# Optimization experiments

Hardware: AMD Instinct MI355X
Metric: run time of the kernel (lower is better)

## Reference

```python
import jax, jax.numpy as jnp
import numpy as np
jax.config.update("jax_enable_x64", True)

WINDOW_SHAPE = (16, 16, 8)
SPARSE_SHAPE = (512, 512, 64)
GROUP_SIZE = 128
BATCH_COUNTS = np.array([500000, 480123, 510007, 495870], dtype=np.int64)  # not multiples of 128 -> padding path active


def setup_inputs() -> dict:
    key = jax.random.key(0)
    kx, ky, kz = jax.random.split(key, 3)
    N = int(BATCH_COUNTS.sum())
    bids = jnp.asarray(np.repeat(np.arange(len(BATCH_COUNTS), dtype=np.int64), BATCH_COUNTS))
    x = jax.random.randint(kx, (N,), 0, SPARSE_SHAPE[0], dtype=jnp.int64)
    y = jax.random.randint(ky, (N,), 0, SPARSE_SHAPE[1], dtype=jnp.int64)
    z = jax.random.randint(kz, (N,), 0, SPARSE_SHAPE[2], dtype=jnp.int64)
    coords = jnp.stack([bids, x, y, z], axis=1)  # [N,4] int64: (batch, x, y, z)
    return {"coords": coords, "batch_size": 4}


def _hash_keys(coords, shifted):
    n, m, l = SPARSE_SHAPE
    n2o, m2o, l2o = WINDOW_SHAPE
    n1 = int(np.ceil(n / n2o) + 1)
    m1 = int(np.ceil(m / m2o) + 1)
    l1 = int(np.ceil(l / l2o) + 1)
    if shifted:
        x = coords[:, 1] + n2o // 2
        y = coords[:, 2] + m2o // 2
        z = coords[:, 3] + l2o // 2
    else:
        x, y, z = coords[:, 1], coords[:, 2], coords[:, 3]
    x1, y1, z1 = x // n2o, y // m2o, z // l2o
    x2, y2, z2 = x % n2o, y % m2o, z % l2o
    # original code triples both window and grid-of-window extents before hashing
    n2, m2, l2 = 3 * n2o, 3 * m2o, 3 * l2o
    n1, m1, l1 = 3 * n1, 3 * m1, 3 * l1
    sx = 1 - 2 * (x1 & 1)  # (-1)**x1
    sy = 1 - 2 * (y1 & 1)
    sz = 1 - 2 * (z1 & 1)
    s2x = 1 - 2 * (x2 & 1)
    s2y = 1 - 2 * (y2 & 1)
    s2z = 1 - 2 * (z2 & 1)
    boff = coords[:, 0] * (n * m * l * 10)
    vx = (n1 * y1 + n1 * m1 * z1 + sy * x1) * (n2 * m2 * l2) + sy * (m2 * x2 + n2 * m2 * z2 + s2x * y2) + boff
    vy = (m1 * z1 + m1 * l1 * x1 + sz * y1) * (m2 * l2 * n2) + sz * (l2 * y2 + m2 * l2 * x2 + s2y * z2) + boff
    vz = (l1 * x1 + l1 * n1 * y1 + sx * z1) * (l2 * n2 * m2) + sx * (n2 * z2 + l2 * n2 * y2 + s2z * x2) + boff
    return vx, vy, vz


def reference(coords, batch_size):
    G = GROUP_SIZE
    coords = coords.astype(jnp.int64)
    bids = coords[:, 0]
    N = coords.shape[0]
    num_per_batch = jax.ops.segment_sum(jnp.ones((N,), jnp.int64), bids, num_segments=batch_size)
    bs = jnp.concatenate([jnp.zeros((1,), jnp.int64), jnp.cumsum(num_per_batch)])
    num_per_batch_p = ((num_per_batch + G - 1) // G) * G
    bsp = jnp.concatenate([jnp.zeros((1,), jnp.int64), jnp.cumsum(num_per_batch_p)])
    Np = int(bsp[-1])  # concrete (not under jit); padded total length

    # win2flat[j] = j + (bsp[b] - bs[b]) for b = batch of element j (coords assumed batch-sorted)
    win2flat = jnp.arange(N, dtype=jnp.int64) + (bsp[:-1] - bs[:-1])[bids]

    # flat2win: identity within each padded batch, with the padded tail replicated
    # from one group earlier, then shifted back to flat indexing.
    p = jnp.arange(Np, dtype=jnp.int64)
    b = jnp.searchsorted(bsp, p, side="right") - 1  # batch of each padded slot
    r = num_per_batch % G
    pad_tail = (r[b] != 0) & (p >= bsp[b + 1] - G + r[b])
    flat2win = p - G * pad_tail.astype(jnp.int64) - (bsp[b] - bs[b])

    outs = [flat2win, win2flat]
    for shifted in (False, True):
        vx, vy, vz = _hash_keys(coords, shifted)
        outs.append(jnp.argsort(vx))
        outs.append(jnp.argsort(vy))
        outs.append(jnp.argsort(vz))
    # (flat2win, win2flat, x, y, z, x_shift, y_shift, z_shift)
    return tuple(outs)
```

## Files before the change

### kernel.cpp

```cpp
#include <hip/hip_runtime.h>
#include <type_traits>

typedef unsigned long long u64;
typedef unsigned int u32;

#define BLOCK     256
#define WAVES     4
#define TILE      4096
#define SUBT      1024
#define CHUNKS    16
#define KSHIFT    21
#define KBIAS     (1LL << 21)
#define KMASK     ((1u << 21) - 1)
#define GRP       128


__device__ __forceinline__ void hash3(long long x, long long y, long long z,
                                      long long boff, long long* v) {
  long long x1 = x >> 4, y1 = y >> 4, z1 = z >> 3;
  long long x2 = x & 15, y2 = y & 15, z2 = z & 7;
  long long sx  = 1 - 2*(x1 & 1), sy  = 1 - 2*(y1 & 1), sz  = 1 - 2*(z1 & 1);
  long long s2x = 1 - 2*(x2 & 1), s2y = 1 - 2*(y2 & 1), s2z = 1 - 2*(z2 & 1);
  v[0] = (99*y1 + 9801*z1 + sy*x1)*55296 + sy*(48*x2 + 2304*z2 + s2x*y2) + boff;
  v[1] = (99*z1 + 2673*x1 + sz*y1)*55296 + sz*(24*y2 + 1152*x2 + s2y*z2) + boff;
  v[2] = (27*x1 + 2673*y1 + sx*z1)*55296 + sx*(48*z2 + 1152*y2 + s2z*x2) + boff;
}

__global__ void count_k(const int* __restrict__ coords, unsigned* __restrict__ counts, int N) {
  __shared__ unsigned c[8];
  if (threadIdx.x < 8) c[threadIdx.x] = 0;
  __syncthreads();
  for (int i = blockIdx.x*blockDim.x + threadIdx.x; i < N; i += gridDim.x*blockDim.x)
    atomicAdd(&c[coords[4*i] & 7], 1u);
  __syncthreads();
  if (threadIdx.x < 8) atomicAdd(&counts[threadIdx.x], c[threadIdx.x]);
}

__global__ void prefix_k(const unsigned* __restrict__ counts, long long* __restrict__ meta,
                         const int* __restrict__ bsz) {
  int NB = *bsz; if (NB > 8) NB = 8;
  long long run_bs = 0, run_bsp = 0;
  meta[0] = 0;
  for (int b = 0; b < NB; b++) {
    long long c  = (long long)counts[b];
    long long cp = (c + GRP - 1) / GRP * GRP;
    long long r  = c % GRP;
    meta[9 + b]  = run_bsp - run_bs;
    meta[17 + b] = r ? (run_bsp + cp - GRP + r) : 0x7fffffffffffffffLL;
    run_bs += c; run_bsp += cp;
    meta[b + 1] = run_bsp;
  }
  meta[25] = run_bsp;
  meta[26] = NB;
}

__global__ void flat2win_k(const long long* __restrict__ meta, int* __restrict__ dout) {
  long long p = (long long)blockIdx.x * blockDim.x + threadIdx.x;
  long long Np = meta[25];
  if (p >= Np) return;
  int NB = (int)meta[26];
  int b = 0;
  while (b < NB - 1 && meta[b + 1] <= p) b++;
  long long pad = (p >= meta[17 + b]) ? 1 : 0;
  dout[p] = (int)(p - GRP * pad - meta[9 + b]);
}

__global__ void __launch_bounds__(BLOCK) keygen_k(const int* __restrict__ coords,
                                                  u64* __restrict__ keys,
                                                  u32* __restrict__ hist,
                                                  const long long* __restrict__ meta,
                                                  int* __restrict__ dout,
                                                  int N, int B, int g0, int g, int doAux) {
  __shared__ u32 cnt[6 * 256];
  int b = blockIdx.x, tid = threadIdx.x;
  int nb = g * 256;
  for (int j = tid; j < nb; j += BLOCK) cnt[j] = 0;
  __syncthreads();
  long long Np = meta[25];
  for (int t = 0; t < CHUNKS; t++) {
    int i = b * TILE + t * BLOCK + tid;
    if (i < N) {
      int4 c4 = ((const int4*)coords)[i];
      long long boff = (long long)c4.x * 167772160LL;
      long long v[6];
      hash3(c4.y,     c4.z,     c4.w,     boff, v);
      hash3(c4.y + 8, c4.z + 8, c4.w + 4, boff, v + 3);
      #pragma unroll
      for (int s = 0; s < 6; s++) {
        if (s >= g0 && s < g0 + g) {
          u64 kb = (u64)(v[s] + KBIAS);
          keys[(size_t)(s - g0) * N + i] = (kb << KSHIFT) | (unsigned)i;
          atomicAdd(&cnt[(s - g0) * 256 + ((unsigned)kb & 255)], 1u);
        }
      }
      if (doAux) dout[Np + i] = (int)(i + meta[9 + c4.x]);
    }
  }
  __syncthreads();
  for (int j = tid; j < nb; j += BLOCK) {
    int s = j >> 8, d = j & 255;
    hist[((size_t)s * B + b) * 256 + d] = cnt[j];
  }
}

template<typename KT, int RADIXN, int SHIFT>
__global__ void __launch_bounds__(BLOCK) hist_k(const KT* __restrict__ src,
                                                u32* __restrict__ hist, int N, int B) {
  __shared__ u32 cnt[RADIXN];
  int s = blockIdx.y, b = blockIdx.x, tid = threadIdx.x;
  for (int j = tid; j < RADIXN; j += BLOCK) cnt[j] = 0;
  __syncthreads();
  const KT* in = src + (size_t)s * N;
  #pragma unroll 4
  for (int t = 0; t < CHUNKS; t++) {
    int i = b * TILE + t * BLOCK + tid;
    if (i < N) {
      unsigned d = (unsigned)(in[i] >> SHIFT) & (RADIXN - 1);
      atomicAdd(&cnt[d], 1u);
    }
  }
  __syncthreads();
  for (int j = tid; j < RADIXN; j += BLOCK) hist[((size_t)s * B + b) * RADIXN + j] = cnt[j];
}

template<int RADIXN>
__global__ void __launch_bounds__(BLOCK) scan_k(u32* __restrict__ hist,
                                                u32* __restrict__ dbase, int B) {
  __shared__ u32 tot[RADIXN];
  int s = blockIdx.x, tid = threadIdx.x;
  for (int d = tid; d < RADIXN; d += BLOCK) {
    u32 run = 0; int b = 0;
    for (; b + 8 <= B; b += 8) {
      u32 v[8];
      #pragma unroll
      for (int j = 0; j < 8; j++) v[j] = hist[((size_t)s * B + b + j) * RADIXN + d];
      #pragma unroll
      for (int j = 0; j < 8; j++) { hist[((size_t)s * B + b + j) * RADIXN + d] = run; run += v[j]; }
    }
    for (; b < B; b++) {
      size_t x = ((size_t)s * B + b) * RADIXN + d;
      u32 v = hist[x]; hist[x] = run; run += v;
    }
    tot[d] = run;
  }
  __syncthreads();
  if (tid < 64) {
    u32 run = 0;
    #pragma unroll
    for (int c = 0; c < RADIXN / 64; c++) {
      u32 v = tot[c * 64 + tid], x = v;
      for (int off = 1; off < 64; off <<= 1) { u32 u = __shfl_up(x, off); if (tid >= off) x += u; }
      dbase[(size_t)s * 512 + c * 64 + tid] = run + x - v;
      run += __shfl(x, 63);
    }
  }
}

template<int RB, int SHIFT, int MODE>
__global__ void __launch_bounds__(BLOCK) scatter_k(const void* __restrict__ srcv,
                                                   void* __restrict__ dstv,
                                                   const u32* __restrict__ hist,
                                                   const u32* __restrict__ dbase,
                                                   int N, int B,
                                                   int* __restrict__ dout,
                                                   const long long* __restrict__ meta, int g0) {
  constexpr int RADIXN = 1 << RB;
  constexpr int DPT = (RADIXN + BLOCK - 1) / BLOCK;
  using KT = typename std::conditional<MODE == 2, u32, u64>::type;
  __shared__ KT items[TILE];
  __shared__ u32 cnt[WAVES][RADIXN];
  __shared__ int exf[RADIXN];
  int s = blockIdx.y, b = blockIdx.x, tid = threadIdx.x;
  int wave = tid >> 6, lane = tid & 63;
  for (int j = tid; j < WAVES * RADIXN; j += BLOCK) ((u32*)cnt)[j] = 0;
  __syncthreads();

  const KT* in = (const KT*)srcv + (size_t)s * N;
  int subbase = b * TILE + wave * SUBT;
  KT k[CHUNKS];
  #pragma unroll
  for (int t = 0; t < CHUNKS; t++) k[t] = in[min(subbase + t * 64 + lane, N - 1)];

  u64 lt = (1ULL << lane) - 1;
  u32 pd[CHUNKS];
  #pragma unroll
  for (int t = 0; t < CHUNKS; t++) {
    int i = subbase + t * 64 + lane;
    bool valid = i < N;
    unsigned d = (unsigned)(k[t] >> SHIFT) & (RADIXN - 1);
    u64 m = __ballot(valid);
    #pragma unroll
    for (int bit = 0; bit < RB; bit++) {
      u64 bal = __ballot(valid && ((d >> bit) & 1));
      m &= ((d >> bit) & 1) ? bal : ~bal;
    }
    u64 below = m & lt;
    unsigned rank = (unsigned)__popcll(below);
    unsigned pbase = cnt[wave][d];
    pd[t] = d | ((pbase + rank) << RB);
    if (valid && below == 0) cnt[wave][d] = pbase + (unsigned)__popcll(m);
  }
  __syncthreads();

  u32 sc[DPT][3];
  #pragma unroll
  for (int q = 0; q < DPT; q++) {
    int d = q * BLOCK + tid;
    u32 a0 = cnt[0][d], a1 = cnt[1][d], a2 = cnt[2][d], a3 = cnt[3][d];
    sc[q][0] = a0; sc[q][1] = a1; sc[q][2] = a2;
    exf[d] = (int)(a0 + a1 + a2 + a3);
  }
  __syncthreads();
  if (tid < 64) {
    u32 run = 0;
    #pragma unroll
    for (int c = 0; c < RADIXN / 64; c++) {
      int dd = c * 64 + tid;
      u32 v = (u32)exf[dd], x = v;
      for (int off = 1; off < 64; off <<= 1) { u32 u = __shfl_up(x, off); if (tid >= off) x += u; }
      exf[dd] = (int)(run + x - v);
      run += __shfl(x, 63);
    }
  }
  __syncthreads();
  const u32* hrow = hist + (size_t)(s * B + b) * RADIXN;
  const u32* brow = dbase + (size_t)s * 512;
  #pragma unroll
  for (int q = 0; q < DPT; q++) {
    int d = q * BLOCK + tid;
    int e = exf[d];
    u32 gb = hrow[d] + brow[d];
    cnt[0][d] = e;
    cnt[1][d] = e + sc[q][0];
    cnt[2][d] = e + sc[q][0] + sc[q][1];
    cnt[3][d] = e + sc[q][0] + sc[q][1] + sc[q][2];
    exf[d] = (int)gb - e;
  }
  __syncthreads();

  #pragma unroll
  for (int t = 0; t < CHUNKS; t++) {
    int i = subbase + t * 64 + lane;
    if (i < N) {
      unsigned d = pd[t] & (RADIXN - 1);
      unsigned lr = pd[t] >> RB;
      items[cnt[wave][d] + lr] = k[t];
    }
  }
  __syncthreads();

  int validCount = N - b * TILE; if (validCount > TILE) validCount = TILE;
  long long obase = 0;
  if (MODE == 2) obase = meta[25] + (long long)N * (1 + g0 + s);
  u64* out64 = (u64*)dstv + (size_t)s * N;
  u32* out32 = (u32*)dstv + (size_t)s * N;
  #pragma unroll 4
  for (int t = 0; t < CHUNKS; t++) {
    int j = t * BLOCK + tid;
    if (j < validCount) {
      KT kk = items[j];
      unsigned d = (unsigned)(kk >> SHIFT) & (RADIXN - 1);
      int gpos = exf[d] + j;
      if constexpr (MODE == 0)      out64[gpos] = kk;
      else if constexpr (MODE == 1) out32[gpos] = (u32)(((kk >> 46) << 21) | (kk & KMASK));
      else                          dout[obase + gpos] = (int)(kk & KMASK);
    }
  }
}

extern "C" void kernel_launch(void* const* d_in, const int* in_sizes, int n_in,
                              void* d_out, int out_size, void* d_ws, size_t ws_size,
                              hipStream_t stream) {
  const int* coords = (const int*)d_in[0];
  const int* bsz    = (const int*)d_in[1];
  int N = in_sizes[0] / 4;
  int* dout = (int*)d_out;
  char* ws = (char*)d_ws;
  int B = (N + TILE - 1) / TILE;

  auto align256 = [](size_t x) { return (x + 255) & ~(size_t)255; };

  int g = 1;
  size_t offHist = 512, offBase = 0, offA = 0, offB = 0;
  const int cands[4] = {6, 3, 2, 1};
  for (int ci = 0; ci < 4; ci++) {
    int cg = cands[ci];
    size_t oBs = offHist + (size_t)cg * B * 512 * 4;
    size_t oA = align256(oBs + (size_t)cg * 512 * 4);
    size_t oB = oA + (size_t)cg * N * 8;
    size_t need = oB + (size_t)cg * N * 8;
    if (need <= ws_size || cg == 1) {
      g = cg; offBase = oBs; offA = oA; offB = oB;
      if (need <= ws_size) break;
    }
  }

  unsigned*  counts = (unsigned*)ws;
  long long* meta   = (long long*)(ws + 64);
  u32*       hist   = (u32*)(ws + offHist);
  u32*       dbase  = (u32*)(ws + offBase);
  u64*       keysA  = (u64*)(ws + offA);
  u64*       keysB  = (u64*)(ws + offB);

  hipMemsetAsync(ws, 0, 512, stream);
  count_k<<<1024, 256, 0, stream>>>(coords, counts, N);
  prefix_k<<<1, 1, 0, stream>>>(counts, meta, bsz);
  flat2win_k<<<(N + 8 * GRP + 255) / 256, 256, 0, stream>>>(meta, dout);

  for (int g0 = 0; g0 < 6; g0 += g) {
    keygen_k<<<B, BLOCK, 0, stream>>>(coords, keysA, hist, meta, dout, N, B, g0, g, g0 == 0);
    scan_k<256><<<g, BLOCK, 0, stream>>>(hist, dbase, B);
    scatter_k<8, 21, 0><<<dim3(B, g), BLOCK, 0, stream>>>(keysA, keysB, hist, dbase, N, B,
                                                          dout, meta, g0);
    hist_k<u64, 256, 29><<<dim3(B, g), BLOCK, 0, stream>>>(keysB, hist, N, B);
    scan_k<256><<<g, BLOCK, 0, stream>>>(hist, dbase, B);
    scatter_k<8, 29, 0><<<dim3(B, g), BLOCK, 0, stream>>>(keysB, keysA, hist, dbase, N, B,
                                                          dout, meta, g0);
    hist_k<u64, 512, 37><<<dim3(B, g), BLOCK, 0, stream>>>(keysA, hist, N, B);
    scan_k<512><<<g, BLOCK, 0, stream>>>(hist, dbase, B);
    scatter_k<9, 37, 1><<<dim3(B, g), BLOCK, 0, stream>>>(keysA, keysB, hist, dbase, N, B,
                                                          dout, meta, g0);
    hist_k<u32, 256, 21><<<dim3(B, g), BLOCK, 0, stream>>>((const u32*)keysB, hist, N, B);
    scan_k<256><<<g, BLOCK, 0, stream>>>(hist, dbase, B);
    scatter_k<8, 21, 2><<<dim3(B, g), BLOCK, 0, stream>>>(keysB, keysA, hist, dbase, N, B,
                                                          dout, meta, g0);
  }
}
```

Baseline: 484.5 us.

## Rebalance radix digit widths to 9/9/9/6 and use 16-bit local counters

Changes the four radix passes from 8/8/9/8-bit digits to 9/9/9/6-bit digits, so the third pass covers more high key bits and the final 32-bit pass sorts only 6 bits. It also generalizes the scan kernels to radices below 64, stores per-wave bucket counters in shared memory as 16-bit values, and adds a fast path for full tiles that skips validity ballots and uses mbcnt for ranking. The intent is to cut ballot work and shared-memory pressure per pass and shrink the last pass's histogram. In exchange, the wider 9-bit digits add ballot iterations and larger histograms in the first two passes.

```diff
diff --git a/kernel.cpp b/kernel.cpp
--- a/kernel.cpp
+++ b/kernel.cpp
@@ -71,9 +71,9 @@
                                                   const long long* __restrict__ meta,
                                                   int* __restrict__ dout,
                                                   int N, int B, int g0, int g, int doAux) {
-  __shared__ u32 cnt[6 * 256];
+  __shared__ u32 cnt[6 * 512];
   int b = blockIdx.x, tid = threadIdx.x;
-  int nb = g * 256;
+  int nb = g * 512;
   for (int j = tid; j < nb; j += BLOCK) cnt[j] = 0;
   __syncthreads();
   long long Np = meta[25];
@@ -90,7 +90,7 @@
         if (s >= g0 && s < g0 + g) {
           u64 kb = (u64)(v[s] + KBIAS);
           keys[(size_t)(s - g0) * N + i] = (kb << KSHIFT) | (unsigned)i;
-          atomicAdd(&cnt[(s - g0) * 256 + ((unsigned)kb & 255)], 1u);
+          atomicAdd(&cnt[(s - g0) * 512 + ((unsigned)kb & 511)], 1u);
         }
       }
       if (doAux) dout[Np + i] = (int)(i + meta[9 + c4.x]);
@@ -98,8 +98,8 @@
   }
   __syncthreads();
   for (int j = tid; j < nb; j += BLOCK) {
-    int s = j >> 8, d = j & 255;
-    hist[((size_t)s * B + b) * 256 + d] = cnt[j];
+    int s = j >> 9, d = j & 511;
+    hist[((size_t)s * B + b) * 512 + d] = cnt[j];
   }
 }
 
@@ -147,10 +147,11 @@
   if (tid < 64) {
     u32 run = 0;
     #pragma unroll
-    for (int c = 0; c < RADIXN / 64; c++) {
-      u32 v = tot[c * 64 + tid], x = v;
+    for (int c = 0; c < RADIXN / 64 || c == 0; c++) {
+      int dd = c * 64 + tid;
+      u32 v = (dd < RADIXN) ? tot[dd] : 0, x = v;
       for (int off = 1; off < 64; off <<= 1) { u32 u = __shfl_up(x, off); if (tid >= off) x += u; }
-      dbase[(size_t)s * 512 + c * 64 + tid] = run + x - v;
+      if (dd < RADIXN) dbase[(size_t)s * 512 + dd] = run + x - v;
       run += __shfl(x, 63);
     }
   }
@@ -168,37 +169,60 @@
   constexpr int DPT = (RADIXN + BLOCK - 1) / BLOCK;
   using KT = typename std::conditional<MODE == 2, u32, u64>::type;
   __shared__ KT items[TILE];
-  __shared__ u32 cnt[WAVES][RADIXN];
+  __shared__ unsigned short cnt[WAVES][RADIXN];
   __shared__ int exf[RADIXN];
   int s = blockIdx.y, b = blockIdx.x, tid = threadIdx.x;
   int wave = tid >> 6, lane = tid & 63;
-  for (int j = tid; j < WAVES * RADIXN; j += BLOCK) ((u32*)cnt)[j] = 0;
+  for (int j = tid; j < WAVES * RADIXN; j += BLOCK) ((unsigned short*)cnt)[j] = 0;
   __syncthreads();
 
   const KT* in = (const KT*)srcv + (size_t)s * N;
   int subbase = b * TILE + wave * SUBT;
+  bool full = (subbase + SUBT <= N);
   KT k[CHUNKS];
-  #pragma unroll
-  for (int t = 0; t < CHUNKS; t++) k[t] = in[min(subbase + t * 64 + lane, N - 1)];
-
-  u64 lt = (1ULL << lane) - 1;
+  if (full) {
+    #pragma unroll
+    for (int t = 0; t < CHUNKS; t++) k[t] = in[subbase + t * 64 + lane];
+  } else {
+    #pragma unroll
+    for (int t = 0; t < CHUNKS; t++) k[t] = in[min(subbase + t * 64 + lane, N - 1)];
+  }
+
   u32 pd[CHUNKS];
-  #pragma unroll
-  for (int t = 0; t < CHUNKS; t++) {
-    int i = subbase + t * 64 + lane;
-    bool valid = i < N;
-    unsigned d = (unsigned)(k[t] >> SHIFT) & (RADIXN - 1);
-    u64 m = __ballot(valid);
-    #pragma unroll
-    for (int bit = 0; bit < RB; bit++) {
-      u64 bal = __ballot(valid && ((d >> bit) & 1));
-      m &= ((d >> bit) & 1) ? bal : ~bal;
-    }
-    u64 below = m & lt;
-    unsigned rank = (unsigned)__popcll(below);
-    unsigned pbase = cnt[wave][d];
-    pd[t] = d | ((pbase + rank) << RB);
-    if (valid && below == 0) cnt[wave][d] = pbase + (unsigned)__popcll(m);
+  if (full) {
+    #pragma unroll
+    for (int t = 0; t < CHUNKS; t++) {
+      unsigned d = (unsigned)(k[t] >> SHIFT) & (RADIXN - 1);
+      u64 m = ~0ull;
+      #pragma unroll
+      for (int bit = 0; bit < RB; bit++) {
+        u64 bal = __ballot((d >> bit) & 1);
+        m &= ((d >> bit) & 1) ? bal : ~bal;
+      }
+      unsigned rank = __builtin_amdgcn_mbcnt_hi((u32)(m >> 32),
+                        __builtin_amdgcn_mbcnt_lo((u32)m, 0u));
+      unsigned pbase = cnt[wave][d];
+      pd[t] = d | ((pbase + rank) << RB);
+      if (rank == 0) cnt[wave][d] = (unsigned short)(pbase + (unsigned)__popcll(m));
+    }
+  } else {
+    #pragma unroll
+    for (int t = 0; t < CHUNKS; t++) {
+      int i = subbase + t * 64 + lane;
+      bool valid = i < N;
+      unsigned d = (unsigned)(k[t] >> SHIFT) & (RADIXN - 1);
+      u64 m = __ballot(valid);
+      #pragma unroll
+      for (int bit = 0; bit < RB; bit++) {
+        u64 bal = __ballot(valid && ((d >> bit) & 1));
+        m &= ((d >> bit) & 1) ? bal : ~bal;
+      }
+      unsigned rank = __builtin_amdgcn_mbcnt_hi((u32)(m >> 32),
+                        __builtin_amdgcn_mbcnt_lo((u32)m, 0u));
+      unsigned pbase = cnt[wave][d];
+      pd[t] = d | ((pbase + rank) << RB);
+      if (valid && rank == 0) cnt[wave][d] = (unsigned short)(pbase + (unsigned)__popcll(m));
+    }
   }
   __syncthreads();
 
@@ -206,19 +230,21 @@
   #pragma unroll
   for (int q = 0; q < DPT; q++) {
     int d = q * BLOCK + tid;
-    u32 a0 = cnt[0][d], a1 = cnt[1][d], a2 = cnt[2][d], a3 = cnt[3][d];
-    sc[q][0] = a0; sc[q][1] = a1; sc[q][2] = a2;
-    exf[d] = (int)(a0 + a1 + a2 + a3);
+    if (d < RADIXN) {
+      u32 a0 = cnt[0][d], a1 = cnt[1][d], a2 = cnt[2][d], a3 = cnt[3][d];
+      sc[q][0] = a0; sc[q][1] = a1; sc[q][2] = a2;
+      exf[d] = (int)(a0 + a1 + a2 + a3);
+    }
   }
   __syncthreads();
   if (tid < 64) {
     u32 run = 0;
     #pragma unroll
-    for (int c = 0; c < RADIXN / 64; c++) {
+    for (int c = 0; c < (RADIXN + 63) / 64; c++) {
       int dd = c * 64 + tid;
-      u32 v = (u32)exf[dd], x = v;
+      u32 v = (dd < RADIXN) ? (u32)exf[dd] : 0, x = v;
       for (int off = 1; off < 64; off <<= 1) { u32 u = __shfl_up(x, off); if (tid >= off) x += u; }
-      exf[dd] = (int)(run + x - v);
+      if (dd < RADIXN) exf[dd] = (int)(run + x - v);
       run += __shfl(x, 63);
     }
   }
@@ -228,13 +254,15 @@
   #pragma unroll
   for (int q = 0; q < DPT; q++) {
     int d = q * BLOCK + tid;
-    int e = exf[d];
-    u32 gb = hrow[d] + brow[d];
-    cnt[0][d] = e;
-    cnt[1][d] = e + sc[q][0];
-    cnt[2][d] = e + sc[q][0] + sc[q][1];
-    cnt[3][d] = e + sc[q][0] + sc[q][1] + sc[q][2];
-    exf[d] = (int)gb - e;
+    if (d < RADIXN) {
+      int e = exf[d];
+      u32 gb = hrow[d] + brow[d];
+      cnt[0][d] = (unsigned short)e;
+      cnt[1][d] = (unsigned short)(e + sc[q][0]);
+      cnt[2][d] = (unsigned short)(e + sc[q][0] + sc[q][1]);
+      cnt[3][d] = (unsigned short)(e + sc[q][0] + sc[q][1] + sc[q][2]);
+      exf[d] = (int)gb - e;
+    }
   }
   __syncthreads();
 
@@ -244,7 +272,7 @@
     if (i < N) {
       unsigned d = pd[t] & (RADIXN - 1);
       unsigned lr = pd[t] >> RB;
-      items[cnt[wave][d] + lr] = k[t];
+      items[(unsigned)cnt[wave][d] + lr] = k[t];
     }
   }
   __syncthreads();
@@ -262,7 +290,7 @@
       unsigned d = (unsigned)(kk >> SHIFT) & (RADIXN - 1);
       int gpos = exf[d] + j;
       if constexpr (MODE == 0)      out64[gpos] = kk;
-      else if constexpr (MODE == 1) out32[gpos] = (u32)(((kk >> 46) << 21) | (kk & KMASK));
+      else if constexpr (MODE == 1) out32[gpos] = (u32)(((kk >> 48) << 21) | (kk & KMASK));
       else                          dout[obase + gpos] = (int)(kk & KMASK);
     }
   }
@@ -309,20 +337,20 @@
 
   for (int g0 = 0; g0 < 6; g0 += g) {
     keygen_k<<<B, BLOCK, 0, stream>>>(coords, keysA, hist, meta, dout, N, B, g0, g, g0 == 0);
-    scan_k<256><<<g, BLOCK, 0, stream>>>(hist, dbase, B);
-    scatter_k<8, 21, 0><<<dim3(B, g), BLOCK, 0, stream>>>(keysA, keysB, hist, dbase, N, B,
+    scan_k<512><<<g, BLOCK, 0, stream>>>(hist, dbase, B);
+    scatter_k<9, 21, 0><<<dim3(B, g), BLOCK, 0, stream>>>(keysA, keysB, hist, dbase, N, B,
                                                           dout, meta, g0);
-    hist_k<u64, 256, 29><<<dim3(B, g), BLOCK, 0, stream>>>(keysB, hist, N, B);
-    scan_k<256><<<g, BLOCK, 0, stream>>>(hist, dbase, B);
-    scatter_k<8, 29, 0><<<dim3(B, g), BLOCK, 0, stream>>>(keysB, keysA, hist, dbase, N, B,
+    hist_k<u64, 512, 30><<<dim3(B, g), BLOCK, 0, stream>>>(keysB, hist, N, B);
+    scan_k<512><<<g, BLOCK, 0, stream>>>(hist, dbase, B);
+    scatter_k<9, 30, 0><<<dim3(B, g), BLOCK, 0, stream>>>(keysB, keysA, hist, dbase, N, B,
                                                           dout, meta, g0);
-    hist_k<u64, 512, 37><<<dim3(B, g), BLOCK, 0, stream>>>(keysA, hist, N, B);
+    hist_k<u64, 512, 39><<<dim3(B, g), BLOCK, 0, stream>>>(keysA, hist, N, B);
     scan_k<512><<<g, BLOCK, 0, stream>>>(hist, dbase, B);
-    scatter_k<9, 37, 1><<<dim3(B, g), BLOCK, 0, stream>>>(keysA, keysB, hist, dbase, N, B,
+    scatter_k<9, 39, 1><<<dim3(B, g), BLOCK, 0, stream>>>(keysA, keysB, hist, dbase, N, B,
                                                           dout, meta, g0);
-    hist_k<u32, 256, 21><<<dim3(B, g), BLOCK, 0, stream>>>((const u32*)keysB, hist, N, B);
-    scan_k<256><<<g, BLOCK, 0, stream>>>(hist, dbase, B);
-    scatter_k<8, 21, 2><<<dim3(B, g), BLOCK, 0, stream>>>(keysB, keysA, hist, dbase, N, B,
+    hist_k<u32, 64, 21><<<dim3(B, g), BLOCK, 0, stream>>>((const u32*)keysB, hist, N, B);
+    scan_k<64><<<g, BLOCK, 0, stream>>>(hist, dbase, B);
+    scatter_k<6, 21, 2><<<dim3(B, g), BLOCK, 0, stream>>>(keysB, keysA, hist, dbase, N, B,
                                                           dout, meta, g0);
   }
 }
```

New measurement: 549.0 us. 1.13x slower.
